# Optimization experiments

Hardware: AMD Instinct MI355X
Metric: run time of the kernel (lower is better)

The kernel has to match this reference:

```python
import jax, jax.numpy as jnp
import numpy as np

N = 100000      # kg_E, number of entities
D = 256         # rel_dim
E = 1600000     # total COO edges (all batches concatenated)


def setup_inputs() -> dict:
    key = jax.random.key(0)
    ks = jax.random.split(key, 8)
    right_embed = jax.random.normal(ks[0], (N, D), dtype=jnp.float32)
    W1 = jax.random.normal(ks[1], (D, D), dtype=jnp.float32) * 0.02
    Wr = jax.random.normal(ks[2], (D, D), dtype=jnp.float32) * 0.02
    br = jax.random.normal(ks[3], (D,), dtype=jnp.float32) * 0.02
    edge_vals = jax.random.uniform(ks[4], (E,), dtype=jnp.float32)  # 1/(deg+1) weights
    edge_rows = jnp.sort(jax.random.randint(ks[5], (E,), 0, N))
    edge_cols = jax.random.randint(ks[6], (E,), 0, N)
    perm = jax.random.randint(ks[7], (N,), 0, N)  # ent_newid_tensor
    return {"right_embed": right_embed, "W1": W1, "Wr": Wr, "br": br,
            "edge_vals": edge_vals, "edge_rows": edge_rows,
            "edge_cols": edge_cols, "perm": perm}


def reference(right_embed, W1, Wr, br, edge_vals, edge_rows, edge_cols, perm):
    # add_diag_layer: dense transform then normalized-adjacency SpMM + ReLU
    h = right_embed @ W1                                   # [N, D]
    msg = edge_vals[:, None] * h[edge_cols]                # [E, D] gather
    agg = jax.ops.segment_sum(msg, edge_rows, num_segments=N)  # scatter-add
    gcn_e_1 = jax.nn.relu(agg)                             # [N, D]
    # highway gate blend with permuted input embeddings
    left = right_embed[perm]                               # [N, D]
    gate = jax.nn.sigmoid(left @ Wr + br)                  # [N, D]
    return gate * gcn_e_1 + (1.0 - gate) * left
```

## Files before the change

### kernel.cpp

```cpp
#include <hip/hip_runtime.h>
#include <hip/hip_bf16.h>
#include <math.h>

#define D 256

typedef short s16x8 __attribute__((ext_vector_type(8)));
typedef float f32x4 __attribute__((ext_vector_type(4)));

__device__ __forceinline__ unsigned short f2bf(float f) {
    unsigned int u = __builtin_bit_cast(unsigned int, f);
    unsigned int r = (u + 0x7fffu + ((u >> 16) & 1u)) >> 16;
    return (unsigned short)r;
}
__device__ __forceinline__ float bf2f(unsigned short s) {
    unsigned int u = ((unsigned int)s) << 16;
    return __builtin_bit_cast(float, u);
}

__global__ void pre_k(const float* __restrict__ W1, const float* __restrict__ Wr,
                      unsigned short* __restrict__ W1sw, unsigned short* __restrict__ Wrsw,
                      const int* __restrict__ rows, int* __restrict__ rp, int N, int E) {
    int bid = blockIdx.x;
    if (bid < 512) {
        int idx = bid * 256 + threadIdx.x;
        int m = idx >> 16;
        int t = idx & 65535;
        const float* src = m ? Wr : W1;
        unsigned short* dst = m ? Wrsw : W1sw;
        int j = t & 7, lane = (t >> 3) & 63, nt = (t >> 9) & 15, kt = t >> 13;
        int k = kt * 32 + (lane >> 4) * 8 + j;
        int n = nt * 16 + (lane & 15);
        dst[t] = f2bf(src[k * D + n]);
    } else {
        int r = (bid - 512) * 256 + threadIdx.x;
        if (r > N) return;
        int lo = 0, hi = E;
        while (lo < hi) {
            int mid = (lo + hi) >> 1;
            if (rows[mid] < r) lo = mid + 1; else hi = mid;
        }
        rp[r] = lo;
    }
}

__device__ __forceinline__ void stage_a_frag(const float* __restrict__ Xrow, int k0,
                                             unsigned short* __restrict__ lA, int fgi) {
    float4 f0 = *(const float4*)(Xrow + k0);
    float4 f1 = *(const float4*)(Xrow + k0 + 4);
    s16x8 sf;
    sf[0] = (short)f2bf(f0.x); sf[1] = (short)f2bf(f0.y);
    sf[2] = (short)f2bf(f0.z); sf[3] = (short)f2bf(f0.w);
    sf[4] = (short)f2bf(f1.x); sf[5] = (short)f2bf(f1.y);
    sf[6] = (short)f2bf(f1.z); sf[7] = (short)f2bf(f1.w);
    *(s16x8*)(lA + (size_t)fgi * 8) = sf;
}

__global__ __launch_bounds__(512) void gemm1_b(const float* __restrict__ X,
                                               const unsigned short* __restrict__ Wsw,
                                               unsigned short* __restrict__ h,
                                               int N, int numTiles) {
    __shared__ unsigned short lA[2 * 8 * 64 * 8];
    int t = threadIdx.x;
    int lane = t & 63;
    int wave = t >> 6;
    int quad = lane >> 4;

    s16x8 bfr[2][8];
#pragma unroll
    for (int ntl = 0; ntl < 2; ntl++) {
        int nt = wave * 2 + ntl;
#pragma unroll
        for (int kt = 0; kt < 8; kt++)
            bfr[ntl][kt] = *(const s16x8*)(Wsw + ((size_t)((kt * 16 + nt) * 64 + lane)) * 8);
    }

    for (int tile = blockIdx.x; tile < numTiles; tile += gridDim.x) {
#pragma unroll
        for (int q = 0; q < 2; q++) {
            int fgi = q * 512 + t;
            int mt = fgi >> 9, kt = (fgi >> 6) & 7, ll = fgi & 63;
            int rl = ll & 15, qd = ll >> 4;
            int grow = tile * 32 + mt * 16 + rl;
            if (grow >= N) grow = N - 1;
            stage_a_frag(X + (size_t)grow * D, kt * 32 + qd * 8, lA, fgi);
        }
        __syncthreads();

        f32x4 acc[2][2];
#pragma unroll
        for (int mt = 0; mt < 2; mt++)
#pragma unroll
            for (int ntl = 0; ntl < 2; ntl++) acc[mt][ntl] = (f32x4){0.f, 0.f, 0.f, 0.f};

#pragma unroll
        for (int mt = 0; mt < 2; mt++)
#pragma unroll
            for (int kt = 0; kt < 8; kt++) {
                s16x8 a = *(const s16x8*)(lA + (size_t)(((mt * 8 + kt) * 64 + lane)) * 8);
                acc[mt][0] = __builtin_amdgcn_mfma_f32_16x16x32_bf16(a, bfr[0][kt], acc[mt][0], 0, 0, 0);
                acc[mt][1] = __builtin_amdgcn_mfma_f32_16x16x32_bf16(a, bfr[1][kt], acc[mt][1], 0, 0, 0);
            }

#pragma unroll
        for (int mt = 0; mt < 2; mt++)
#pragma unroll
            for (int ntl = 0; ntl < 2; ntl++) {
                int col = (wave * 2 + ntl) * 16 + (lane & 15);
#pragma unroll
                for (int r = 0; r < 4; r++) {
                    int grow = tile * 32 + mt * 16 + quad * 4 + r;
                    if (grow < N) h[(size_t)grow * D + col] = f2bf(acc[mt][ntl][r]);
                }
            }
        __syncthreads();
    }
}

__device__ __forceinline__ void acc4(float4& a, uint2 u, float v) {
    float x0 = __builtin_bit_cast(float, u.x << 16);
    float x1 = __builtin_bit_cast(float, u.x & 0xffff0000u);
    float x2 = __builtin_bit_cast(float, u.y << 16);
    float x3 = __builtin_bit_cast(float, u.y & 0xffff0000u);
    a.x += v * x0; a.y += v * x1; a.z += v * x2; a.w += v * x3;
}

__global__ __launch_bounds__(512, 4) void gemm2_f(const float* __restrict__ X,
                                                  const int* __restrict__ perm,
                                                  const unsigned short* __restrict__ Wsw,
                                                  const float* __restrict__ br,
                                                  const uint2* __restrict__ hp,
                                                  const int* __restrict__ rp,
                                                  const int* __restrict__ cols,
                                                  const float* __restrict__ vals,
                                                  float* __restrict__ out,
                                                  int N, int E, int numTiles) {
    __shared__ unsigned short lA[2 * 8 * 64 * 8];
    __shared__ __attribute__((aligned(16))) float lAgg[32][260];
    int t = threadIdx.x;
    int lane = t & 63;
    int wave = t >> 6;
    int quad = lane >> 4;
    int tile = blockIdx.x;
    if (tile >= numTiles) return;

#pragma unroll
    for (int q = 0; q < 2; q++) {
        int fgi = q * 512 + t;
        int mt = fgi >> 9, kt = (fgi >> 6) & 7, ll = fgi & 63;
        int rl = ll & 15, qd = ll >> 4;
        int grow = tile * 32 + mt * 16 + rl;
        if (grow >= N) grow = N - 1;
        int pr = perm[grow];
        stage_a_frag(X + (size_t)pr * D, kt * 32 + qd * 8, lA, fgi);
    }

    s16x8 bfr[2][8];
#pragma unroll
    for (int ntl = 0; ntl < 2; ntl++) {
        int nt = wave * 2 + ntl;
#pragma unroll
        for (int kt = 0; kt < 8; kt++)
            bfr[ntl][kt] = *(const s16x8*)(Wsw + ((size_t)((kt * 16 + nt) * 64 + lane)) * 8);
    }
    __syncthreads();

    f32x4 acc[2][2];
#pragma unroll
    for (int mt = 0; mt < 2; mt++)
#pragma unroll
        for (int ntl = 0; ntl < 2; ntl++) acc[mt][ntl] = (f32x4){0.f, 0.f, 0.f, 0.f};

#pragma unroll
    for (int mt = 0; mt < 2; mt++)
#pragma unroll
        for (int kt = 0; kt < 8; kt++) {
            s16x8 a = *(const s16x8*)(lA + (size_t)(((mt * 8 + kt) * 64 + lane)) * 8);
            acc[mt][0] = __builtin_amdgcn_mfma_f32_16x16x32_bf16(a, bfr[0][kt], acc[mt][0], 0, 0, 0);
            acc[mt][1] = __builtin_amdgcn_mfma_f32_16x16x32_bf16(a, bfr[1][kt], acc[mt][1], 0, 0, 0);
        }

#pragma unroll 1
    for (int rr = 0; rr < 4; rr++) {
        int row = tile * 32 + wave * 4 + rr;
        if (row >= N) break;
        int start = rp[row], end = rp[row + 1];
        float4 a = {0.f, 0.f, 0.f, 0.f};
        for (int base = start; base < end; base += 64) {
            int ii = base + lane;
            int iic = ii < E ? ii : E - 1;
            int cl = cols[iic];
            int vbits = __builtin_bit_cast(int, vals[iic]);
            int n = end - base; if (n > 64) n = 64;
            int i = 0;
            for (; i + 8 <= n; i += 8) {
                uint2 u[8]; float vv[8];
#pragma unroll
                for (int k = 0; k < 8; k++) {
                    int c = __builtin_amdgcn_readlane(cl, i + k);
                    vv[k] = __builtin_bit_cast(float, __builtin_amdgcn_readlane(vbits, i + k));
                    u[k] = hp[(size_t)c * 64 + lane];
                }
#pragma unroll
                for (int k = 0; k < 8; k++) acc4(a, u[k], vv[k]);
            }
            for (; i < n; i++) {
                int c = __builtin_amdgcn_readlane(cl, i);
                float v = __builtin_bit_cast(float, __builtin_amdgcn_readlane(vbits, i));
                uint2 u = hp[(size_t)c * 64 + lane];
                acc4(a, u, v);
            }
        }
        a.x = fmaxf(a.x, 0.f); a.y = fmaxf(a.y, 0.f);
        a.z = fmaxf(a.z, 0.f); a.w = fmaxf(a.w, 0.f);
        *(float4*)(&lAgg[wave * 4 + rr][lane * 4]) = a;
    }
    __syncthreads();

#pragma unroll
    for (int mt = 0; mt < 2; mt++) {
#pragma unroll
        for (int ntl = 0; ntl < 2; ntl++) {
            int col = (wave * 2 + ntl) * 16 + (lane & 15);
            float b = br[col];
            int kt2 = col >> 5, qd2 = (col >> 3) & 3, j2 = col & 7;
#pragma unroll
            for (int r = 0; r < 4; r++) {
                int rt = mt * 16 + quad * 4 + r;
                int grow = tile * 32 + rt;
                if (grow < N) {
                    float pre = acc[mt][ntl][r] + b;
                    float gate = 1.f / (1.f + __expf(-pre));
                    float gcn = lAgg[rt][col];
                    float left = bf2f(lA[(size_t)(((mt * 8 + kt2) * 64 + qd2 * 16 + (rt & 15))) * 8 + j2]);
                    out[(size_t)grow * D + col] = gate * gcn + (1.f - gate) * left;
                }
            }
        }
    }
}

extern "C" void kernel_launch(void* const* d_in, const int* in_sizes, int n_in,
                              void* d_out, int out_size, void* d_ws, size_t ws_size,
                              hipStream_t stream) {
    const float* right = (const float*)d_in[0];
    const float* W1    = (const float*)d_in[1];
    const float* Wr    = (const float*)d_in[2];
    const float* br    = (const float*)d_in[3];
    const float* evals = (const float*)d_in[4];
    const int*   erows = (const int*)d_in[5];
    const int*   ecols = (const int*)d_in[6];
    const int*   perm  = (const int*)d_in[7];
    int N = in_sizes[7];
    int E = in_sizes[4];
    float* out = (float*)d_out;

    char* ws = (char*)d_ws;
    unsigned short* W1sw = (unsigned short*)ws;
    unsigned short* Wrsw = W1sw + D * D;
    int* rp = (int*)(ws + (size_t)2 * D * D * 2);
    size_t off = (size_t)2 * D * D * 2 + 4 * (size_t)(N + 1);
    off = (off + 255) & ~(size_t)255;
    unsigned short* h = (unsigned short*)(ws + off);

    int numTiles = (N + 31) / 32;
    int rpBlocks = (N + 256) / 256;

    pre_k<<<512 + rpBlocks, 256, 0, stream>>>(W1, Wr, W1sw, Wrsw, erows, rp, N, E);
    gemm1_b<<<numTiles, 512, 0, stream>>>(right, W1sw, h, N, numTiles);
    gemm2_f<<<numTiles, 512, 0, stream>>>(right, perm, Wrsw, br, (const uint2*)h,
                                          rp, ecols, evals, out, N, E, numTiles);
}
```

Before: 403.2 us.

## Reorder SpMM before W1 GEMM and fuse both GEMMs into one kernel

Uses associativity, A·(X·W1) = (A·X)·W1, to aggregate the bf16-converted input embeddings first in a dedicated scatter kernel, then apply W1 and Wr in a single fused GEMM/gate kernel. A new pre-pass converts X to bf16 once, so the gathers and the permuted-left staging read half-size rows. This removes the separate gemm1 launch and the large LDS aggregation buffer in the gate kernel. In exchange the aggregated result is rounded to bf16 before the matmul, which adds precision loss, and the full bf16 copy of X must be written and read back.

```diff
diff --git a/kernel.cpp b/kernel.cpp
--- a/kernel.cpp
+++ b/kernel.cpp
@@ -17,9 +17,12 @@
     return __builtin_bit_cast(float, u);
 }
 
-__global__ void pre_k(const float* __restrict__ W1, const float* __restrict__ Wr,
-                      unsigned short* __restrict__ W1sw, unsigned short* __restrict__ Wrsw,
-                      const int* __restrict__ rows, int* __restrict__ rp, int N, int E) {
+__global__ void pre_all(const float* __restrict__ X,
+                        const float* __restrict__ W1, const float* __restrict__ Wr,
+                        unsigned short* __restrict__ Xbf,
+                        unsigned short* __restrict__ W1sw, unsigned short* __restrict__ Wrsw,
+                        const int* __restrict__ rows, int* __restrict__ rp,
+                        int N, int E, int rpBlocks) {
     int bid = blockIdx.x;
     if (bid < 512) {
         int idx = bid * 256 + threadIdx.x;
@@ -31,7 +34,7 @@
         int k = kt * 32 + (lane >> 4) * 8 + j;
         int n = nt * 16 + (lane & 15);
         dst[t] = f2bf(src[k * D + n]);
-    } else {
+    } else if (bid < 512 + rpBlocks) {
         int r = (bid - 512) * 256 + threadIdx.x;
         if (r > N) return;
         int lo = 0, hi = E;
@@ -40,79 +43,18 @@
             if (rows[mid] < r) lo = mid + 1; else hi = mid;
         }
         rp[r] = lo;
-    }
-}
-
-__device__ __forceinline__ void stage_a_frag(const float* __restrict__ Xrow, int k0,
-                                             unsigned short* __restrict__ lA, int fgi) {
-    float4 f0 = *(const float4*)(Xrow + k0);
-    float4 f1 = *(const float4*)(Xrow + k0 + 4);
-    s16x8 sf;
-    sf[0] = (short)f2bf(f0.x); sf[1] = (short)f2bf(f0.y);
-    sf[2] = (short)f2bf(f0.z); sf[3] = (short)f2bf(f0.w);
-    sf[4] = (short)f2bf(f1.x); sf[5] = (short)f2bf(f1.y);
-    sf[6] = (short)f2bf(f1.z); sf[7] = (short)f2bf(f1.w);
-    *(s16x8*)(lA + (size_t)fgi * 8) = sf;
-}
-
-__global__ __launch_bounds__(512) void gemm1_b(const float* __restrict__ X,
-                                               const unsigned short* __restrict__ Wsw,
-                                               unsigned short* __restrict__ h,
-                                               int N, int numTiles) {
-    __shared__ unsigned short lA[2 * 8 * 64 * 8];
-    int t = threadIdx.x;
-    int lane = t & 63;
-    int wave = t >> 6;
-    int quad = lane >> 4;
-
-    s16x8 bfr[2][8];
-#pragma unroll
-    for (int ntl = 0; ntl < 2; ntl++) {
-        int nt = wave * 2 + ntl;
-#pragma unroll
-        for (int kt = 0; kt < 8; kt++)
-            bfr[ntl][kt] = *(const s16x8*)(Wsw + ((size_t)((kt * 16 + nt) * 64 + lane)) * 8);
-    }
-
-    for (int tile = blockIdx.x; tile < numTiles; tile += gridDim.x) {
-#pragma unroll
-        for (int q = 0; q < 2; q++) {
-            int fgi = q * 512 + t;
-            int mt = fgi >> 9, kt = (fgi >> 6) & 7, ll = fgi & 63;
-            int rl = ll & 15, qd = ll >> 4;
-            int grow = tile * 32 + mt * 16 + rl;
-            if (grow >= N) grow = N - 1;
-            stage_a_frag(X + (size_t)grow * D, kt * 32 + qd * 8, lA, fgi);
-        }
-        __syncthreads();
-
-        f32x4 acc[2][2];
-#pragma unroll
-        for (int mt = 0; mt < 2; mt++)
-#pragma unroll
-            for (int ntl = 0; ntl < 2; ntl++) acc[mt][ntl] = (f32x4){0.f, 0.f, 0.f, 0.f};
-
-#pragma unroll
-        for (int mt = 0; mt < 2; mt++)
-#pragma unroll
-            for (int kt = 0; kt < 8; kt++) {
-                s16x8 a = *(const s16x8*)(lA + (size_t)(((mt * 8 + kt) * 64 + lane)) * 8);
-                acc[mt][0] = __builtin_amdgcn_mfma_f32_16x16x32_bf16(a, bfr[0][kt], acc[mt][0], 0, 0, 0);
-                acc[mt][1] = __builtin_amdgcn_mfma_f32_16x16x32_bf16(a, bfr[1][kt], acc[mt][1], 0, 0, 0);
-            }
-
-#pragma unroll
-        for (int mt = 0; mt < 2; mt++)
-#pragma unroll
-            for (int ntl = 0; ntl < 2; ntl++) {
-                int col = (wave * 2 + ntl) * 16 + (lane & 15);
-#pragma unroll
-                for (int r = 0; r < 4; r++) {
-                    int grow = tile * 32 + mt * 16 + quad * 4 + r;
-                    if (grow < N) h[(size_t)grow * D + col] = f2bf(acc[mt][ntl][r]);
-                }
-            }
-        __syncthreads();
+    } else {
+        long long c = (long long)(bid - 512 - rpBlocks) * 256 + threadIdx.x;
+        long long i8 = c * 8;
+        if (i8 >= (long long)N * D) return;
+        float4 f0 = *(const float4*)(X + i8);
+        float4 f1 = *(const float4*)(X + i8 + 4);
+        s16x8 sf;
+        sf[0] = (short)f2bf(f0.x); sf[1] = (short)f2bf(f0.y);
+        sf[2] = (short)f2bf(f0.z); sf[3] = (short)f2bf(f0.w);
+        sf[4] = (short)f2bf(f1.x); sf[5] = (short)f2bf(f1.y);
+        sf[6] = (short)f2bf(f1.z); sf[7] = (short)f2bf(f1.w);
+        *(s16x8*)(Xbf + i8) = sf;
     }
 }
 
@@ -124,18 +66,59 @@
     a.x += v * x0; a.y += v * x1; a.z += v * x2; a.w += v * x3;
 }
 
-__global__ __launch_bounds__(512, 4) void gemm2_f(const float* __restrict__ X,
+__global__ __launch_bounds__(256) void scatter_x(const uint2* __restrict__ xp,
+                                                 const int* __restrict__ rp,
+                                                 const int* __restrict__ cols,
+                                                 const float* __restrict__ vals,
+                                                 uint2* __restrict__ aggp,
+                                                 int N, int E) {
+    int lane = threadIdx.x & 63;
+    int wave = threadIdx.x >> 6;
+    int row = blockIdx.x * 4 + wave;
+    if (row >= N) return;
+    int start = rp[row], end = rp[row + 1];
+
+    float4 a = {0.f, 0.f, 0.f, 0.f};
+    for (int base = start; base < end; base += 64) {
+        int ii = base + lane;
+        int iic = ii < E ? ii : E - 1;
+        int cl = cols[iic];
+        int vbits = __builtin_bit_cast(int, vals[iic]);
+        int n = end - base; if (n > 64) n = 64;
+        int i = 0;
+        for (; i + 8 <= n; i += 8) {
+            uint2 u[8]; float vv[8];
+#pragma unroll
+            for (int k = 0; k < 8; k++) {
+                int c = __builtin_amdgcn_readlane(cl, i + k);
+                vv[k] = __builtin_bit_cast(float, __builtin_amdgcn_readlane(vbits, i + k));
+                u[k] = xp[(size_t)c * 64 + lane];
+            }
+#pragma unroll
+            for (int k = 0; k < 8; k++) acc4(a, u[k], vv[k]);
+        }
+        for (; i < n; i++) {
+            int c = __builtin_amdgcn_readlane(cl, i);
+            float v = __builtin_bit_cast(float, __builtin_amdgcn_readlane(vbits, i));
+            uint2 u = xp[(size_t)c * 64 + lane];
+            acc4(a, u, v);
+        }
+    }
+    uint2 o;
+    o.x = (unsigned int)f2bf(a.x) | ((unsigned int)f2bf(a.y) << 16);
+    o.y = (unsigned int)f2bf(a.z) | ((unsigned int)f2bf(a.w) << 16);
+    aggp[(size_t)row * 64 + lane] = o;
+}
+
+__global__ __launch_bounds__(512, 4) void gemm_ff(const unsigned short* __restrict__ aggX,
+                                                  const unsigned short* __restrict__ Xbf,
                                                   const int* __restrict__ perm,
-                                                  const unsigned short* __restrict__ Wsw,
+                                                  const unsigned short* __restrict__ W1sw,
+                                                  const unsigned short* __restrict__ Wrsw,
                                                   const float* __restrict__ br,
-                                                  const uint2* __restrict__ hp,
-                                                  const int* __restrict__ rp,
-                                                  const int* __restrict__ cols,
-                                                  const float* __restrict__ vals,
                                                   float* __restrict__ out,
-                                                  int N, int E, int numTiles) {
-    __shared__ unsigned short lA[2 * 8 * 64 * 8];
-    __shared__ __attribute__((aligned(16))) float lAgg[32][260];
+                                                  int N, int numTiles) {
+    __shared__ unsigned short lA[8 * 64 * 16];
     int t = threadIdx.x;
     int lane = t & 63;
     int wave = t >> 6;
@@ -151,7 +134,7 @@
         int grow = tile * 32 + mt * 16 + rl;
         if (grow >= N) grow = N - 1;
         int pr = perm[grow];
-        stage_a_frag(X + (size_t)pr * D, kt * 32 + qd * 8, lA, fgi);
+        *(s16x8*)(lA + (size_t)fgi * 8) = *(const s16x8*)(Xbf + (size_t)pr * D + kt * 32 + qd * 8);
     }
 
     s16x8 bfr[2][8];
@@ -160,61 +143,49 @@
         int nt = wave * 2 + ntl;
 #pragma unroll
         for (int kt = 0; kt < 8; kt++)
-            bfr[ntl][kt] = *(const s16x8*)(Wsw + ((size_t)((kt * 16 + nt) * 64 + lane)) * 8);
+            bfr[ntl][kt] = *(const s16x8*)(W1sw + ((size_t)((kt * 16 + nt) * 64 + lane)) * 8);
+    }
+    f32x4 acc1[2][2];
+#pragma unroll
+    for (int mt = 0; mt < 2; mt++)
+#pragma unroll
+        for (int ntl = 0; ntl < 2; ntl++) acc1[mt][ntl] = (f32x4){0.f, 0.f, 0.f, 0.f};
+
+#pragma unroll
+    for (int mt = 0; mt < 2; mt++) {
+        int grow = tile * 32 + mt * 16 + (lane & 15);
+        if (grow >= N) grow = N - 1;
+        const unsigned short* ap = aggX + (size_t)grow * D + (lane >> 4) * 8;
+#pragma unroll
+        for (int kt = 0; kt < 8; kt++) {
+            s16x8 a = *(const s16x8*)(ap + kt * 32);
+            acc1[mt][0] = __builtin_amdgcn_mfma_f32_16x16x32_bf16(a, bfr[0][kt], acc1[mt][0], 0, 0, 0);
+            acc1[mt][1] = __builtin_amdgcn_mfma_f32_16x16x32_bf16(a, bfr[1][kt], acc1[mt][1], 0, 0, 0);
+        }
     }
     __syncthreads();
 
-    f32x4 acc[2][2];
+#pragma unroll
+    for (int ntl = 0; ntl < 2; ntl++) {
+        int nt = wave * 2 + ntl;
+#pragma unroll
+        for (int kt = 0; kt < 8; kt++)
+            bfr[ntl][kt] = *(const s16x8*)(Wrsw + ((size_t)((kt * 16 + nt) * 64 + lane)) * 8);
+    }
+    f32x4 acc2[2][2];
 #pragma unroll
     for (int mt = 0; mt < 2; mt++)
 #pragma unroll
-        for (int ntl = 0; ntl < 2; ntl++) acc[mt][ntl] = (f32x4){0.f, 0.f, 0.f, 0.f};
+        for (int ntl = 0; ntl < 2; ntl++) acc2[mt][ntl] = (f32x4){0.f, 0.f, 0.f, 0.f};
 
 #pragma unroll
     for (int mt = 0; mt < 2; mt++)
 #pragma unroll
         for (int kt = 0; kt < 8; kt++) {
             s16x8 a = *(const s16x8*)(lA + (size_t)(((mt * 8 + kt) * 64 + lane)) * 8);
-            acc[mt][0] = __builtin_amdgcn_mfma_f32_16x16x32_bf16(a, bfr[0][kt], acc[mt][0], 0, 0, 0);
-            acc[mt][1] = __builtin_amdgcn_mfma_f32_16x16x32_bf16(a, bfr[1][kt], acc[mt][1], 0, 0, 0);
-        }
-
-#pragma unroll 1
-    for (int rr = 0; rr < 4; rr++) {
-        int row = tile * 32 + wave * 4 + rr;
-        if (row >= N) break;
-        int start = rp[row], end = rp[row + 1];
-        float4 a = {0.f, 0.f, 0.f, 0.f};
-        for (int base = start; base < end; base += 64) {
-            int ii = base + lane;
-            int iic = ii < E ? ii : E - 1;
-            int cl = cols[iic];
-            int vbits = __builtin_bit_cast(int, vals[iic]);
-            int n = end - base; if (n > 64) n = 64;
-            int i = 0;
-            for (; i + 8 <= n; i += 8) {
-                uint2 u[8]; float vv[8];
-#pragma unroll
-                for (int k = 0; k < 8; k++) {
-                    int c = __builtin_amdgcn_readlane(cl, i + k);
-                    vv[k] = __builtin_bit_cast(float, __builtin_amdgcn_readlane(vbits, i + k));
-                    u[k] = hp[(size_t)c * 64 + lane];
-                }
-#pragma unroll
-                for (int k = 0; k < 8; k++) acc4(a, u[k], vv[k]);
-            }
-            for (; i < n; i++) {
-                int c = __builtin_amdgcn_readlane(cl, i);
-                float v = __builtin_bit_cast(float, __builtin_amdgcn_readlane(vbits, i));
-                uint2 u = hp[(size_t)c * 64 + lane];
-                acc4(a, u, v);
-            }
-        }
-        a.x = fmaxf(a.x, 0.f); a.y = fmaxf(a.y, 0.f);
-        a.z = fmaxf(a.z, 0.f); a.w = fmaxf(a.w, 0.f);
-        *(float4*)(&lAgg[wave * 4 + rr][lane * 4]) = a;
-    }
-    __syncthreads();
+            acc2[mt][0] = __builtin_amdgcn_mfma_f32_16x16x32_bf16(a, bfr[0][kt], acc2[mt][0], 0, 0, 0);
+            acc2[mt][1] = __builtin_amdgcn_mfma_f32_16x16x32_bf16(a, bfr[1][kt], acc2[mt][1], 0, 0, 0);
+        }
 
 #pragma unroll
     for (int mt = 0; mt < 2; mt++) {
@@ -228,9 +199,9 @@
                 int rt = mt * 16 + quad * 4 + r;
                 int grow = tile * 32 + rt;
                 if (grow < N) {
-                    float pre = acc[mt][ntl][r] + b;
+                    float pre = acc2[mt][ntl][r] + b;
                     float gate = 1.f / (1.f + __expf(-pre));
-                    float gcn = lAgg[rt][col];
+                    float gcn = fmaxf(acc1[mt][ntl][r], 0.f);
                     float left = bf2f(lA[(size_t)(((mt * 8 + kt2) * 64 + qd2 * 16 + (rt & 15))) * 8 + j2]);
                     out[(size_t)grow * D + col] = gate * gcn + (1.f - gate) * left;
                 }
@@ -260,13 +231,17 @@
     int* rp = (int*)(ws + (size_t)2 * D * D * 2);
     size_t off = (size_t)2 * D * D * 2 + 4 * (size_t)(N + 1);
     off = (off + 255) & ~(size_t)255;
-    unsigned short* h = (unsigned short*)(ws + off);
+    unsigned short* Xbf = (unsigned short*)(ws + off);
+    unsigned short* aggX = Xbf + (size_t)N * D;
 
     int numTiles = (N + 31) / 32;
     int rpBlocks = (N + 256) / 256;
-
-    pre_k<<<512 + rpBlocks, 256, 0, stream>>>(W1, Wr, W1sw, Wrsw, erows, rp, N, E);
-    gemm1_b<<<numTiles, 512, 0, stream>>>(right, W1sw, h, N, numTiles);
-    gemm2_f<<<numTiles, 512, 0, stream>>>(right, perm, Wrsw, br, (const uint2*)h,
-                                          rp, ecols, evals, out, N, E, numTiles);
-}
+    long long cvtElems = (long long)N * D / 8;
+    int cvtBlocks = (int)((cvtElems + 255) / 256);
+
+    pre_all<<<512 + rpBlocks + cvtBlocks, 256, 0, stream>>>(right, W1, Wr, Xbf, W1sw, Wrsw,
+                                                            erows, rp, N, E, rpBlocks);
+    scatter_x<<<(N + 3) / 4, 256, 0, stream>>>((const uint2*)Xbf, rp, ecols, evals,
+                                               (uint2*)aggX, N, E);
+    gemm_ff<<<numTiles, 512, 0, stream>>>(aggX, Xbf, perm, W1sw, Wrsw, br, out, N, numTiles);
+}
```

After: 395.1 us. -2.0%, faster.
